# Optimization experiments

Hardware: AMD Instinct MI355X
Metric: run time of the kernel (lower is better)

## Reference

```python
import jax, jax.numpy as jnp
import numpy as np

EPS = 1e-6


def setup_inputs() -> dict:
    key = jax.random.key(0)
    kx, kw = jax.random.split(key)
    B, C, N = 8, 256, 2048
    x = jax.random.normal(kx, (B, C, N), dtype=jnp.float32)
    # nn.Linear(dim*2, 2, bias=False): weight shape [2, 2*C]
    W = jax.random.normal(kw, (2, 2 * C), dtype=jnp.float32) * (1.0 / np.sqrt(2 * C))
    return {"x": x, "W": W}


def reference(x, W):
    B, C, N = x.shape
    # cosine similarity matrix [B, N, N]
    sim = jnp.einsum('bcn,bcm->bnm', x, x)
    # torch: sqrt(sum(x^2 + 1e-6, dim=1)) -> eps added per-channel before sum
    norms = jnp.sqrt(jnp.sum(x * x + EPS, axis=1))            # [B, N]
    io_abs = sim / (norms[:, :, None] * norms[:, None, :])    # [B, N, N]
    # zero the diagonal (fill_diagonal_(0)) before argmax
    io_abs = io_abs * (1.0 - jnp.eye(N, dtype=io_abs.dtype))
    idx = jnp.argmax(io_abs, axis=2)                          # [B, N] nearest-neighbor per token
    # gather retrieved features: f_re[b, :, n] = x[b, :, idx[b, n]]
    f_re = jnp.take_along_axis(x, idx[:, None, :], axis=2)    # [B, C, N]
    # gated fusion
    fus = jnp.concatenate([x, f_re], axis=1).transpose(0, 2, 1)  # [B, N, 2C]
    w = jax.nn.softmax(fus @ W.T, axis=-1)                    # [B, N, 2]
    w = w.transpose(0, 2, 1)                                  # [B, 2, N]
    out = x * w[:, 0:1, :] + f_re * w[:, 1:2, :]
    return (out, f_re)
```

## Files before the change

kernel.cpp:

```cpp
#include <hip/hip_runtime.h>
#include <hip/hip_bf16.h>
#include <math.h>

constexpr int B_ = 8;
constexpr int C_ = 256;
constexpr int N_ = 2048;
constexpr int CN_ = C_ * N_;
constexpr int TOT_ = B_ * C_ * N_;
constexpr int BN_ = B_ * N_;
constexpr int NTILES = 16;
constexpr int NPAIRS = 136;
constexpr float EPSC = 256.0f * 1e-6f;

typedef __attribute__((ext_vector_type(8))) short bf16x8;
typedef __attribute__((ext_vector_type(4))) float f32x4;
typedef __attribute__((ext_vector_type(2))) unsigned int u32x2;

__device__ __forceinline__ void g2l16(const void* g, void* l) {
    __builtin_amdgcn_global_load_lds(
        (const __attribute__((address_space(1))) void*)g,
        (__attribute__((address_space(3))) void*)l, 16, 0, 0);
}

__device__ __forceinline__ unsigned short bits(__hip_bfloat16 h) {
    union { __hip_bfloat16 b; unsigned short u; } cv;
    cv.b = h;
    return cv.u;
}

__device__ __forceinline__ float b2f(short s) {
    union { float f; unsigned u; } cv;
    cv.u = ((unsigned)(unsigned short)s) << 16;
    return cv.f;
}

__device__ __forceinline__ unsigned long long packkey(float v, int m) {
    const unsigned b = __float_as_uint(v);
    const unsigned u = (b & 0x80000000u) ? ~b : (b | 0x80000000u);
    return ((unsigned long long)u << 32) | (unsigned)(2047 - m);
}

__device__ __forceinline__ float rnorm4(const float* __restrict__ normp, int idx) {
    return 1.0f / sqrtf(normp[idx] + EPSC);
}

__device__ __forceinline__ unsigned packpair(float a, float b) {
    return ((unsigned)bits(__float2bfloat16(b)) << 16) | bits(__float2bfloat16(a));
}

__global__ __launch_bounds__(256) void convert_kernel(const float* __restrict__ x,
                                                      __hip_bfloat16* __restrict__ hiT,
                                                      __hip_bfloat16* __restrict__ loT,
                                                      float* __restrict__ normp,
                                                      int* __restrict__ rcnt) {
    const int blk = blockIdx.x;
    const int batch = blk & 7;
    const int nt = (blk >> 3) & 31;
    const int ctile = blk >> 8;
    const int n0 = nt << 6, c0 = ctile << 6;
    const int t = threadIdx.x;

    if (blk == 0 && t == 0) rcnt[0] = 0;

    __shared__ float tb[64][65];
    __shared__ float red[16][65];

    const int i4 = t & 15;
    const int j = t >> 4;
    const float* xp = x + (size_t)batch * CN_ + (size_t)c0 * N_ + n0;
#pragma unroll
    for (int p = 0; p < 4; ++p) {
        const int cl = j + p * 16;
        const float4 v = *(const float4*)(xp + (size_t)cl * N_ + 4 * i4);
        tb[cl][4 * i4 + 0] = v.x;
        tb[cl][4 * i4 + 1] = v.y;
        tb[cl][4 * i4 + 2] = v.z;
        tb[cl][4 * i4 + 3] = v.w;
    }
    __syncthreads();

    const int cq = t & 15;
    const int nb = t >> 4;
    const int c = cq << 2;
#pragma unroll
    for (int r = 0; r < 4; ++r) {
        const int n = nb + r * 16;
        const float v0 = tb[c][n], v1 = tb[c + 1][n];
        const float v2 = tb[c + 2][n], v3 = tb[c + 3][n];
        const __hip_bfloat16 h0 = __float2bfloat16(v0);
        const __hip_bfloat16 h1 = __float2bfloat16(v1);
        const __hip_bfloat16 h2 = __float2bfloat16(v2);
        const __hip_bfloat16 h3 = __float2bfloat16(v3);
        const float g0 = v0 - __bfloat162float(h0);
        const float g1 = v1 - __bfloat162float(h1);
        const float g2 = v2 - __bfloat162float(h2);
        const float g3 = v3 - __bfloat162float(h3);
        red[cq][n] = v0 * v0 + v1 * v1 + v2 * v2 + v3 * v3;
        const size_t o = ((size_t)batch * N_ + n0 + n) * C_ + c0 + c;
        u32x2 hp, lp;
        hp[0] = ((unsigned)bits(h1) << 16) | bits(h0);
        hp[1] = ((unsigned)bits(h3) << 16) | bits(h2);
        lp[0] = packpair(g0, g1);
        lp[1] = packpair(g2, g3);
        ((u32x2*)hiT)[o >> 2] = hp;
        ((u32x2*)loT)[o >> 2] = lp;
        __syncthreads();
    }
    if (t < 64) {
        float s = 0.f;
#pragma unroll
        for (int g = 0; g < 16; ++g) s += red[g][t];
        normp[ctile * BN_ + batch * N_ + n0 + t] = s;
    }
}

__device__ __forceinline__ float rnormsum(const float* __restrict__ normp, int idx) {
    return 1.0f / sqrtf(normp[idx] + normp[BN_ + idx] + normp[2 * BN_ + idx] +
                        normp[3 * BN_ + idx] + EPSC);
}

__global__ __launch_bounds__(512) void gram_mfma_kernel(
        const __hip_bfloat16* __restrict__ hiT, const __hip_bfloat16* __restrict__ loT,
        const float* __restrict__ normp,
        float* __restrict__ pval, int* __restrict__ pidx, float* __restrict__ pval2) {
    const int blk = blockIdx.x;
    const int batch = blk & 7;
    int p = blk >> 3;
    int bn = 0;
    while (p >= NTILES - bn) { p -= NTILES - bn; ++bn; }
    const int bm = bn + p;
    const bool diag = (bn == bm);
    const int n0 = bn << 7, m0 = bm << 7;

    __shared__ short As0[128 * 64];
    __shared__ short As1[128 * 64];
    __shared__ short Bs0[128 * 64];
    __shared__ short Bs1[128 * 64];
    short* ov = &As0[0];
    float (*rv1)[4] = (float(*)[4])(ov + 0);
    int (*ri1)[4] = (int(*)[4])(ov + 1024);
    float (*rv2)[4] = (float(*)[4])(ov + 2048);
    float (*cv1)[2] = (float(*)[2])(ov + 3072);
    int (*ci1)[2] = (int(*)[2])(ov + 3584);
    float (*cv2)[2] = (float(*)[2])(ov + 4096);
    float* rnA = (float*)(ov + 4608);

    const int tid = threadIdx.x;
    const int l = tid & 63, w = tid >> 6;
    const int lm = l & 15, q = l >> 4;
    const int x7 = lm & 7;
    const int wn = (w >> 2) << 6;
    const int wm = (w & 3) << 5;

    const size_t bbase = (size_t)batch * CN_;
    const short* gA[2];
    const short* gB[2];
    int ldsoff[2];
#pragma unroll
    for (int pp = 0; pp < 2; ++pp) {
        const int slot = tid + pp * 512;
        const int r = slot >> 3, sidx = slot & 7;
        const int sw = sidx ^ (r & 7);
        const short* base = (const short*)((sw < 4) ? hiT : loT);
        gA[pp] = base + bbase + (size_t)(n0 + r) * C_ + (sw & 3) * 8;
        gB[pp] = base + bbase + (size_t)(m0 + r) * C_ + (sw & 3) * 8;
        ldsoff[pp] = slot * 8;
    }
    int aoff[8], boff[4];
#pragma unroll
    for (int rt = 0; rt < 4; ++rt) {
        const int ra = wn + rt * 16 + lm;
        aoff[rt * 2] = ra * 64 + ((q ^ x7) * 8);
        aoff[rt * 2 + 1] = ra * 64 + (((4 | q) ^ x7) * 8);
    }
#pragma unroll
    for (int ct = 0; ct < 2; ++ct) {
        const int rb = wm + ct * 16 + lm;
        boff[ct * 2] = rb * 64 + ((q ^ x7) * 8);
        boff[ct * 2 + 1] = rb * 64 + (((4 | q) ^ x7) * 8);
    }

    f32x4 acc[4][2];
#pragma unroll
    for (int rt = 0; rt < 4; ++rt)
#pragma unroll
        for (int ct = 0; ct < 2; ++ct) acc[rt][ct] = (f32x4){0.f, 0.f, 0.f, 0.f};

#pragma unroll
    for (int pp = 0; pp < 2; ++pp) {
        g2l16(gA[pp], As0 + ldsoff[pp]);
        g2l16(gB[pp], Bs0 + ldsoff[pp]);
    }
    __syncthreads();

#pragma unroll
    for (int kt = 0; kt < 8; ++kt) {
        short* Ac = (kt & 1) ? As1 : As0;
        short* Bc = (kt & 1) ? Bs1 : Bs0;
        if (kt < 7) {
            short* An = (kt & 1) ? As0 : As1;
            short* Bn = (kt & 1) ? Bs0 : Bs1;
#pragma unroll
            for (int pp = 0; pp < 2; ++pp) {
                g2l16(gA[pp] + (kt + 1) * 32, An + ldsoff[pp]);
                g2l16(gB[pp] + (kt + 1) * 32, Bn + ldsoff[pp]);
            }
        }
        bf16x8 ah[4], al[4], bh[2], bl[2];
#pragma unroll
        for (int rt = 0; rt < 4; ++rt) {
            ah[rt] = *(const bf16x8*)(Ac + aoff[rt * 2]);
            al[rt] = *(const bf16x8*)(Ac + aoff[rt * 2 + 1]);
        }
#pragma unroll
        for (int ct = 0; ct < 2; ++ct) {
            bh[ct] = *(const bf16x8*)(Bc + boff[ct * 2]);
            bl[ct] = *(const bf16x8*)(Bc + boff[ct * 2 + 1]);
        }
#pragma unroll
        for (int rt = 0; rt < 4; ++rt)
#pragma unroll
            for (int ct = 0; ct < 2; ++ct) {
                acc[rt][ct] = __builtin_amdgcn_mfma_f32_16x16x32_bf16(
                    ah[rt], bh[ct], acc[rt][ct], 0, 0, 0);
                acc[rt][ct] = __builtin_amdgcn_mfma_f32_16x16x32_bf16(
                    ah[rt], bl[ct], acc[rt][ct], 0, 0, 0);
                acc[rt][ct] = __builtin_amdgcn_mfma_f32_16x16x32_bf16(
                    al[rt], bh[ct], acc[rt][ct], 0, 0, 0);
            }
        __syncthreads();
    }

    if (tid < 128) rnA[tid] = rnormsum(normp, batch * N_ + n0 + tid);

    float rnm[2];
#pragma unroll
    for (int ct = 0; ct < 2; ++ct)
        rnm[ct] = rnormsum(normp, batch * N_ + m0 + wm + ct * 16 + lm);

#pragma unroll
    for (int rt = 0; rt < 4; ++rt) {
#pragma unroll
        for (int r = 0; r < 4; ++r) {
            const int nrow = n0 + wn + rt * 16 + q * 4 + r;
            float v1 = -3.4e38f, v2 = -3.4e38f;
            int i1 = 0x7fffffff;
#pragma unroll
            for (int ct = 0; ct < 2; ++ct) {
                const int m = m0 + wm + ct * 16 + lm;
                const float v = acc[rt][ct][r] * rnm[ct];
                if (m == nrow) continue;
                if (v > v1) { v2 = v1; v1 = v; i1 = m; }
                else if (v > v2) v2 = v;
            }
#pragma unroll
            for (int d = 1; d < 16; d <<= 1) {
                const float ov1 = __shfl_xor(v1, d, 64);
                const int oi1 = __shfl_xor(i1, d, 64);
                const float ov2 = __shfl_xor(v2, d, 64);
                if (ov1 > v1 || (ov1 == v1 && oi1 < i1)) {
                    v2 = fmaxf(v1, ov2); v1 = ov1; i1 = oi1;
                } else {
                    v2 = fmaxf(v2, ov1);
                }
            }
            if (lm == 0) {
                const int rloc = wn + rt * 16 + q * 4 + r;
                rv1[rloc][w & 3] = v1;
                ri1[rloc][w & 3] = i1;
                rv2[rloc][w & 3] = v2;
            }
        }
    }
    __syncthreads();

    if (!diag) {
        float rnn[4][4];
#pragma unroll
        for (int rt = 0; rt < 4; ++rt)
#pragma unroll
            for (int r = 0; r < 4; ++r) rnn[rt][r] = rnA[wn + rt * 16 + q * 4 + r];
#pragma unroll
        for (int ct = 0; ct < 2; ++ct) {
            float v1 = -3.4e38f, v2 = -3.4e38f;
            int i1 = 0x7fffffff;
#pragma unroll
            for (int rt = 0; rt < 4; ++rt) {
#pragma unroll
                for (int r = 0; r < 4; ++r) {
                    const float v = acc[rt][ct][r] * rnn[rt][r];
                    const int nn = n0 + wn + rt * 16 + q * 4 + r;
                    if (v > v1) { v2 = v1; v1 = v; i1 = nn; }
                    else if (v > v2) v2 = v;
                }
            }
#pragma unroll
            for (int d = 16; d < 64; d <<= 1) {
                const float ov1 = __shfl_xor(v1, d, 64);
                const int oi1 = __shfl_xor(i1, d, 64);
                const float ov2 = __shfl_xor(v2, d, 64);
                if (ov1 > v1 || (ov1 == v1 && oi1 < i1)) {
                    v2 = fmaxf(v1, ov2); v1 = ov1; i1 = oi1;
                } else {
                    v2 = fmaxf(v2, ov1);
                }
            }
            if (q == 0) {
                const int mloc = wm + ct * 16 + lm;
                cv1[mloc][w >> 2] = v1;
                ci1[mloc][w >> 2] = i1;
                cv2[mloc][w >> 2] = v2;
            }
        }
    }
    __syncthreads();

    if (tid < 128) {
        {
            float v1 = rv1[tid][0]; int i1 = ri1[tid][0]; float v2 = rv2[tid][0];
#pragma unroll
            for (int s = 1; s < 4; ++s) {
                const float ov1 = rv1[tid][s]; const int oi1 = ri1[tid][s]; const float ov2 = rv2[tid][s];
                if (ov1 > v1 || (ov1 == v1 && oi1 < i1)) { v2 = fmaxf(v1, ov2); v1 = ov1; i1 = oi1; }
                else v2 = fmaxf(v2, ov1);
            }
            const size_t gi = (size_t)(batch * NTILES + bm) * N_ + n0 + tid;
            pval[gi] = v1; pidx[gi] = i1; pval2[gi] = v2;
        }
        if (!diag) {
            float v1 = cv1[tid][0]; int i1 = ci1[tid][0]; float v2 = cv2[tid][0];
            const float ov1 = cv1[tid][1]; const int oi1 = ci1[tid][1]; const float ov2 = cv2[tid][1];
            if (ov1 > v1 || (ov1 == v1 && oi1 < i1)) { v2 = fmaxf(v1, ov2); v1 = ov1; i1 = oi1; }
            else v2 = fmaxf(v2, ov1);
            const size_t gi = (size_t)(batch * NTILES + bn) * N_ + m0 + tid;
            pval[gi] = v1; pidx[gi] = i1; pval2[gi] = v2;
        }
    }
}

__global__ void combine_kernel(const float* __restrict__ pval, const int* __restrict__ pidx,
                               const float* __restrict__ pval2, int* __restrict__ fidx,
                               int* __restrict__ rcnt, int* __restrict__ ridx,
                               unsigned long long* __restrict__ pbest) {
    const int gt = blockIdx.x * 256 + threadIdx.x;
    const int row = gt >> 2, part = gt & 3;
    const int batch = row >> 11, n = row & 2047;
    float v1 = -3.4e38f, v2 = -3.4e38f;
    int i1 = 0x7fffffff;
    for (int s = part; s < NTILES; s += 4) {
        const size_t gi = (size_t)(batch * NTILES + s) * N_ + n;
        const float ov1 = pval[gi]; const int oi1 = pidx[gi]; const float ov2 = pval2[gi];
        if (ov1 > v1 || (ov1 == v1 && oi1 < i1)) { v2 = fmaxf(v1, ov2); v1 = ov1; i1 = oi1; }
        else v2 = fmaxf(v2, ov1);
    }
#pragma unroll
    for (int d = 1; d < 4; d <<= 1) {
        const float ov1 = __shfl_xor(v1, d, 64);
        const int oi1 = __shfl_xor(i1, d, 64);
        const float ov2 = __shfl_xor(v2, d, 64);
        if (ov1 > v1 || (ov1 == v1 && oi1 < i1)) { v2 = fmaxf(v1, ov2); v1 = ov1; i1 = oi1; }
        else v2 = fmaxf(v2, ov1);
    }
    if (part == 0) {
        fidx[row] = i1;
        if (v1 - v2 < 4e-5f) {
            const int slot = atomicAdd(rcnt, 1);
            ridx[slot] = row;
            pbest[slot] = 0ull;
        }
    }
}

__global__ __launch_bounds__(256) void rescue_kernel(const float* __restrict__ x,
                                                     const float* __restrict__ normp,
                                                     const int* __restrict__ rcnt,
                                                     const int* __restrict__ ridx,
                                                     unsigned long long* __restrict__ pbest) {
    const int cnt = *rcnt;
    const int nwork = cnt << 3;
    const int tid = threadIdx.x;
    __shared__ unsigned long long bk[256];
    for (int wi = blockIdx.x; wi < nwork; wi += gridDim.x) {
        const int rr = wi >> 3, ch = wi & 7;
        const int t = ridx[rr];
        const int batch = t >> 11, n = t & 2047;
        const int m = (ch << 8) + tid;
        const float* xb = x + (size_t)batch * CN_;
        float s0 = 0.f, s1 = 0.f, s2 = 0.f, s3 = 0.f;
        const float* xn = xb + n;
        const float* xm = xb + m;
#pragma unroll 4
        for (int c = 0; c < C_; c += 4) {
            s0 += xn[(size_t)(c + 0) * N_] * xm[(size_t)(c + 0) * N_];
            s1 += xn[(size_t)(c + 1) * N_] * xm[(size_t)(c + 1) * N_];
            s2 += xn[(size_t)(c + 2) * N_] * xm[(size_t)(c + 2) * N_];
            s3 += xn[(size_t)(c + 3) * N_] * xm[(size_t)(c + 3) * N_];
        }
        const float v = ((s0 + s1) + (s2 + s3)) * rnormsum(normp, batch * N_ + m);
        bk[tid] = (m == n) ? 0ull : packkey(v, m);
        __syncthreads();
        for (int sft = 128; sft > 0; sft >>= 1) {
            if (tid < sft) {
                const unsigned long long o = bk[tid + sft];
                if (o > bk[tid]) bk[tid] = o;
            }
            __syncthreads();
        }
        if (tid == 0) atomicMax(&pbest[rr], bk[0]);
        __syncthreads();
    }
}

__global__ __launch_bounds__(512) void finish_kernel(const float* __restrict__ x,
                                                     const __hip_bfloat16* __restrict__ hiT,
                                                     const __hip_bfloat16* __restrict__ loT,
                                                     const float* __restrict__ W,
                                                     const int* __restrict__ fidx,
                                                     const int* __restrict__ rcnt,
                                                     const int* __restrict__ ridx,
                                                     const unsigned long long* __restrict__ pbest,
                                                     float* __restrict__ out) {
    const int batch = blockIdx.x & 7;
    const int nt = blockIdx.x >> 3;
    const int n0 = nt << 4;
    const int t = threadIdx.x;
    const int i = t & 15, cg = t >> 4;

    __shared__ float Wl[1024];
    __shared__ int il[16];
    __shared__ float pl0[32][17], pl1[32][17];
    __shared__ float w0s[16], w1s[16];

    for (int u = t; u < 1024; u += 512) Wl[u] = W[u];
    if (t < 16) il[t] = fidx[batch * N_ + n0 + t];
    __syncthreads();
    {
        const int cnt = *rcnt;
        for (int rr = t; rr < cnt; rr += 512) {
            const int tt = ridx[rr];
            if ((tt >> 11) == batch) {
                const int n = tt & 2047;
                if (n >= n0 && n < n0 + 16) {
                    const unsigned long long k = pbest[rr];
                    il[n - n0] = 2047 - (int)(unsigned)(k & 0xffffffffull);
                }
            }
        }
    }
    __syncthreads();

    const int myrow = il[i];
    const size_t rowb = ((size_t)batch * N_ + myrow) * C_ + cg * 8;

    float fre[8];
    {
        const bf16x8 h = *(const bf16x8*)(hiT + rowb);
        const bf16x8 g = *(const bf16x8*)(loT + rowb);
#pragma unroll
        for (int e = 0; e < 8; ++e) fre[e] = b2f(h[e]) + b2f(g[e]);
    }

    const float* xb = x + (size_t)batch * CN_ + n0 + i;
    float xr[8];
    float l0 = 0.f, l1 = 0.f;
#pragma unroll
    for (int cc = 0; cc < 8; ++cc) {
        const int c = cg * 8 + cc;
        const float xv = xb[(size_t)c * N_];
        xr[cc] = xv;
        l0 += xv * Wl[c] + fre[cc] * Wl[256 + c];
        l1 += xv * Wl[512 + c] + fre[cc] * Wl[768 + c];
    }
    pl0[cg][i] = l0;
    pl1[cg][i] = l1;
    __syncthreads();
    if (t < 16) {
        float L0 = 0.f, L1 = 0.f;
#pragma unroll
        for (int g = 0; g < 32; ++g) { L0 += pl0[g][t]; L1 += pl1[g][t]; }
        const float mx = fmaxf(L0, L1);
        const float e0 = expf(L0 - mx);
        const float e1 = expf(L1 - mx);
        const float inv = 1.0f / (e0 + e1);
        w0s[t] = e0 * inv;
        w1s[t] = e1 * inv;
    }
    __syncthreads();
    const float w0 = w0s[i], w1 = w1s[i];

#pragma unroll
    for (int cc = 0; cc < 8; ++cc) {
        const int c = cg * 8 + cc;
        const size_t off = (size_t)batch * CN_ + (size_t)c * N_ + n0 + i;
        __builtin_nontemporal_store(xr[cc] * w0 + fre[cc] * w1, out + off);
        __builtin_nontemporal_store(fre[cc], out + TOT_ + off);
    }
}

extern "C" void kernel_launch(void* const* d_in, const int* in_sizes, int n_in,
                              void* d_out, int out_size, void* d_ws, size_t ws_size,
                              hipStream_t stream) {
    const float* x = (const float*)d_in[0];
    const float* W = (const float*)d_in[1];
    float* out = (float*)d_out;

    const size_t BF_BYTES = (size_t)TOT_ * 2;
    const size_t NORM_BYTES = (size_t)BN_ * 4;
    const size_t P_BYTES = (size_t)B_ * NTILES * N_ * 4;

    uint8_t* p = (uint8_t*)d_ws;
    __hip_bfloat16* hiT = (__hip_bfloat16*)p; p += BF_BYTES;
    __hip_bfloat16* loT = (__hip_bfloat16*)p; p += BF_BYTES;
    float* normp = (float*)p; p += 4 * NORM_BYTES;
    float* pval = (float*)p; p += P_BYTES;
    int* pidx = (int*)p; p += P_BYTES;
    float* pval2 = (float*)p; p += P_BYTES;
    int* fidx = (int*)p; p += NORM_BYTES;
    int* rcnt = (int*)p; p += 256;
    int* ridx = (int*)p; p += NORM_BYTES;
    unsigned long long* pbest = (unsigned long long*)p; p += (size_t)BN_ * 8;

    convert_kernel<<<1024, 256, 0, stream>>>(x, hiT, loT, normp, rcnt);
    gram_mfma_kernel<<<B_ * NPAIRS, 512, 0, stream>>>(hiT, loT, normp, pval, pidx, pval2);
    combine_kernel<<<256, 256, 0, stream>>>(pval, pidx, pval2, fidx, rcnt, ridx, pbest);
    rescue_kernel<<<2048, 256, 0, stream>>>(x, normp, rcnt, ridx, pbest);
    finish_kernel<<<1024, 512, 0, stream>>>(x, hiT, loT, W, fidx, rcnt, ridx, pbest, out);
}
```

Before: 166.2 us.

## Enlarge Gram tiles to 256x256, drop double buffering, shuffle-reduce norms

Doubles the Gram block tile to 256x256 with a 128x64 per-warp sub-tile, cutting block count and partial argmax outputs so each loaded tile is reused more. Replaces the double-buffered async LDS prefetch with a single buffer and barriers on both sides of each k-step. The convert kernel now reduces per-column norms with wave shuffles instead of an LDS array and per-iteration barriers. Risks include lost load/compute overlap, higher register pressure and fewer blocks than CUs.

After: 192.5 us. 15.8% more time.

```diff
diff --git a/kernel.cpp b/kernel.cpp
--- a/kernel.cpp
+++ b/kernel.cpp
@@ -8,8 +8,8 @@
 constexpr int CN_ = C_ * N_;
 constexpr int TOT_ = B_ * C_ * N_;
 constexpr int BN_ = B_ * N_;
-constexpr int NTILES = 16;
-constexpr int NPAIRS = 136;
+constexpr int NT2 = 8;
+constexpr int NP2 = 36;
 constexpr float EPSC = 256.0f * 1e-6f;
 
 typedef __attribute__((ext_vector_type(8))) short bf16x8;
@@ -40,12 +40,13 @@
     return ((unsigned long long)u << 32) | (unsigned)(2047 - m);
 }
 
-__device__ __forceinline__ float rnorm4(const float* __restrict__ normp, int idx) {
-    return 1.0f / sqrtf(normp[idx] + EPSC);
-}
-
 __device__ __forceinline__ unsigned packpair(float a, float b) {
     return ((unsigned)bits(__float2bfloat16(b)) << 16) | bits(__float2bfloat16(a));
+}
+
+__device__ __forceinline__ float rnormsum(const float* __restrict__ normp, int idx) {
+    return 1.0f / sqrtf(normp[idx] + normp[BN_ + idx] + normp[2 * BN_ + idx] +
+                        normp[3 * BN_ + idx] + EPSC);
 }
 
 __global__ __launch_bounds__(256) void convert_kernel(const float* __restrict__ x,
@@ -63,7 +64,6 @@
     if (blk == 0 && t == 0) rcnt[0] = 0;
 
     __shared__ float tb[64][65];
-    __shared__ float red[16][65];
 
     const int i4 = t & 15;
     const int j = t >> 4;
@@ -95,7 +95,6 @@
         const float g1 = v1 - __bfloat162float(h1);
         const float g2 = v2 - __bfloat162float(h2);
         const float g3 = v3 - __bfloat162float(h3);
-        red[cq][n] = v0 * v0 + v1 * v1 + v2 * v2 + v3 * v3;
         const size_t o = ((size_t)batch * N_ + n0 + n) * C_ + c0 + c;
         u32x2 hp, lp;
         hp[0] = ((unsigned)bits(h1) << 16) | bits(h0);
@@ -104,19 +103,11 @@
         lp[1] = packpair(g2, g3);
         ((u32x2*)hiT)[o >> 2] = hp;
         ((u32x2*)loT)[o >> 2] = lp;
-        __syncthreads();
-    }
-    if (t < 64) {
-        float s = 0.f;
-#pragma unroll
-        for (int g = 0; g < 16; ++g) s += red[g][t];
-        normp[ctile * BN_ + batch * N_ + n0 + t] = s;
-    }
-}
-
-__device__ __forceinline__ float rnormsum(const float* __restrict__ normp, int idx) {
-    return 1.0f / sqrtf(normp[idx] + normp[BN_ + idx] + normp[2 * BN_ + idx] +
-                        normp[3 * BN_ + idx] + EPSC);
+        float nrm = v0 * v0 + v1 * v1 + v2 * v2 + v3 * v3;
+#pragma unroll
+        for (int d = 1; d < 16; d <<= 1) nrm += __shfl_xor(nrm, d, 64);
+        if (cq == 0) normp[ctile * BN_ + batch * N_ + n0 + n] = nrm;
+    }
 }
 
 __global__ __launch_bounds__(512) void gram_mfma_kernel(
@@ -127,37 +118,35 @@
     const int batch = blk & 7;
     int p = blk >> 3;
     int bn = 0;
-    while (p >= NTILES - bn) { p -= NTILES - bn; ++bn; }
+    while (p >= NT2 - bn) { p -= NT2 - bn; ++bn; }
     const int bm = bn + p;
     const bool diag = (bn == bm);
-    const int n0 = bn << 7, m0 = bm << 7;
-
-    __shared__ short As0[128 * 64];
-    __shared__ short As1[128 * 64];
-    __shared__ short Bs0[128 * 64];
-    __shared__ short Bs1[128 * 64];
-    short* ov = &As0[0];
+    const int n0 = bn << 8, m0 = bm << 8;
+
+    __shared__ short As[256 * 64];
+    __shared__ short Bs[256 * 64];
+    short* ov = &As[0];
     float (*rv1)[4] = (float(*)[4])(ov + 0);
-    int (*ri1)[4] = (int(*)[4])(ov + 1024);
-    float (*rv2)[4] = (float(*)[4])(ov + 2048);
-    float (*cv1)[2] = (float(*)[2])(ov + 3072);
-    int (*ci1)[2] = (int(*)[2])(ov + 3584);
-    float (*cv2)[2] = (float(*)[2])(ov + 4096);
-    float* rnA = (float*)(ov + 4608);
+    int (*ri1)[4] = (int(*)[4])(ov + 2048);
+    float (*rv2)[4] = (float(*)[4])(ov + 4096);
+    float (*cv1)[2] = (float(*)[2])(ov + 6144);
+    int (*ci1)[2] = (int(*)[2])(ov + 7168);
+    float (*cv2)[2] = (float(*)[2])(ov + 8192);
+    float* rnA = (float*)(ov + 9216);
 
     const int tid = threadIdx.x;
     const int l = tid & 63, w = tid >> 6;
     const int lm = l & 15, q = l >> 4;
     const int x7 = lm & 7;
-    const int wn = (w >> 2) << 6;
-    const int wm = (w & 3) << 5;
+    const int wn = (w >> 2) << 7;
+    const int wm = (w & 3) << 6;
 
     const size_t bbase = (size_t)batch * CN_;
-    const short* gA[2];
-    const short* gB[2];
-    int ldsoff[2];
-#pragma unroll
-    for (int pp = 0; pp < 2; ++pp) {
+    const short* gA[4];
+    const short* gB[4];
+    int ldsoff[4];
+#pragma unroll
+    for (int pp = 0; pp < 4; ++pp) {
         const int slot = tid + pp * 512;
         const int r = slot >> 3, sidx = slot & 7;
         const int sw = sidx ^ (r & 7);
@@ -166,87 +155,73 @@
         gB[pp] = base + bbase + (size_t)(m0 + r) * C_ + (sw & 3) * 8;
         ldsoff[pp] = slot * 8;
     }
-    int aoff[8], boff[4];
-#pragma unroll
-    for (int rt = 0; rt < 4; ++rt) {
+    int aoffh[8], aoffl[8], boffh[4], boffl[4];
+#pragma unroll
+    for (int rt = 0; rt < 8; ++rt) {
         const int ra = wn + rt * 16 + lm;
-        aoff[rt * 2] = ra * 64 + ((q ^ x7) * 8);
-        aoff[rt * 2 + 1] = ra * 64 + (((4 | q) ^ x7) * 8);
-    }
-#pragma unroll
-    for (int ct = 0; ct < 2; ++ct) {
+        aoffh[rt] = ra * 64 + ((q ^ x7) * 8);
+        aoffl[rt] = ra * 64 + (((4 | q) ^ x7) * 8);
+    }
+#pragma unroll
+    for (int ct = 0; ct < 4; ++ct) {
         const int rb = wm + ct * 16 + lm;
-        boff[ct * 2] = rb * 64 + ((q ^ x7) * 8);
-        boff[ct * 2 + 1] = rb * 64 + (((4 | q) ^ x7) * 8);
-    }
-
-    f32x4 acc[4][2];
-#pragma unroll
-    for (int rt = 0; rt < 4; ++rt)
-#pragma unroll
-        for (int ct = 0; ct < 2; ++ct) acc[rt][ct] = (f32x4){0.f, 0.f, 0.f, 0.f};
-
-#pragma unroll
-    for (int pp = 0; pp < 2; ++pp) {
-        g2l16(gA[pp], As0 + ldsoff[pp]);
-        g2l16(gB[pp], Bs0 + ldsoff[pp]);
-    }
-    __syncthreads();
-
-#pragma unroll
+        boffh[ct] = rb * 64 + ((q ^ x7) * 8);
+        boffl[ct] = rb * 64 + (((4 | q) ^ x7) * 8);
+    }
+
+    f32x4 acc[8][4];
+#pragma unroll
+    for (int rt = 0; rt < 8; ++rt)
+#pragma unroll
+        for (int ct = 0; ct < 4; ++ct) acc[rt][ct] = (f32x4){0.f, 0.f, 0.f, 0.f};
+
     for (int kt = 0; kt < 8; ++kt) {
-        short* Ac = (kt & 1) ? As1 : As0;
-        short* Bc = (kt & 1) ? Bs1 : Bs0;
-        if (kt < 7) {
-            short* An = (kt & 1) ? As0 : As1;
-            short* Bn = (kt & 1) ? Bs0 : Bs1;
-#pragma unroll
-            for (int pp = 0; pp < 2; ++pp) {
-                g2l16(gA[pp] + (kt + 1) * 32, An + ldsoff[pp]);
-                g2l16(gB[pp] + (kt + 1) * 32, Bn + ldsoff[pp]);
-            }
-        }
-        bf16x8 ah[4], al[4], bh[2], bl[2];
-#pragma unroll
-        for (int rt = 0; rt < 4; ++rt) {
-            ah[rt] = *(const bf16x8*)(Ac + aoff[rt * 2]);
-            al[rt] = *(const bf16x8*)(Ac + aoff[rt * 2 + 1]);
-        }
-#pragma unroll
-        for (int ct = 0; ct < 2; ++ct) {
-            bh[ct] = *(const bf16x8*)(Bc + boff[ct * 2]);
-            bl[ct] = *(const bf16x8*)(Bc + boff[ct * 2 + 1]);
-        }
-#pragma unroll
-        for (int rt = 0; rt < 4; ++rt)
-#pragma unroll
-            for (int ct = 0; ct < 2; ++ct) {
+        __syncthreads();
+#pragma unroll
+        for (int pp = 0; pp < 4; ++pp) {
+            g2l16(gA[pp] + kt * 32, As + ldsoff[pp]);
+            g2l16(gB[pp] + kt * 32, Bs + ldsoff[pp]);
+        }
+        __syncthreads();
+        bf16x8 bh[4], bl[4];
+#pragma unroll
+        for (int ct = 0; ct < 4; ++ct) {
+            bh[ct] = *(const bf16x8*)(Bs + boffh[ct]);
+            bl[ct] = *(const bf16x8*)(Bs + boffl[ct]);
+        }
+#pragma unroll
+        for (int rt = 0; rt < 8; ++rt) {
+            const bf16x8 ah = *(const bf16x8*)(As + aoffh[rt]);
+            const bf16x8 al = *(const bf16x8*)(As + aoffl[rt]);
+#pragma unroll
+            for (int ct = 0; ct < 4; ++ct) {
                 acc[rt][ct] = __builtin_amdgcn_mfma_f32_16x16x32_bf16(
-                    ah[rt], bh[ct], acc[rt][ct], 0, 0, 0);
+                    ah, bh[ct], acc[rt][ct], 0, 0, 0);
                 acc[rt][ct] = __builtin_amdgcn_mfma_f32_16x16x32_bf16(
-                    ah[rt], bl[ct], acc[rt][ct], 0, 0, 0);
+                    ah, bl[ct], acc[rt][ct], 0, 0, 0);
                 acc[rt][ct] = __builtin_amdgcn_mfma_f32_16x16x32_bf16(
-                    al[rt], bh[ct], acc[rt][ct], 0, 0, 0);
-            }
-        __syncthreads();
-    }
-
-    if (tid < 128) rnA[tid] = rnormsum(normp, batch * N_ + n0 + tid);
-
-    float rnm[2];
-#pragma unroll
-    for (int ct = 0; ct < 2; ++ct)
+                    al, bh[ct], acc[rt][ct], 0, 0, 0);
+            }
+        }
+    }
+    __syncthreads();
+
+    if (tid < 256) rnA[tid] = rnormsum(normp, batch * N_ + n0 + tid);
+
+    float rnm[4];
+#pragma unroll
+    for (int ct = 0; ct < 4; ++ct)
         rnm[ct] = rnormsum(normp, batch * N_ + m0 + wm + ct * 16 + lm);
 
 #pragma unroll
-    for (int rt = 0; rt < 4; ++rt) {
+    for (int rt = 0; rt < 8; ++rt) {
 #pragma unroll
         for (int r = 0; r < 4; ++r) {
             const int nrow = n0 + wn + rt * 16 + q * 4 + r;
             float v1 = -3.4e38f, v2 = -3.4e38f;
             int i1 = 0x7fffffff;
 #pragma unroll
-            for (int ct = 0; ct < 2; ++ct) {
+            for (int ct = 0; ct < 4; ++ct) {
                 const int m = m0 + wm + ct * 16 + lm;
                 const float v = acc[rt][ct][r] * rnm[ct];
                 if (m == nrow) continue;
@@ -275,20 +250,15 @@
     __syncthreads();
 
     if (!diag) {
-        float rnn[4][4];
-#pragma unroll
-        for (int rt = 0; rt < 4; ++rt)
-#pragma unroll
-            for (int r = 0; r < 4; ++r) rnn[rt][r] = rnA[wn + rt * 16 + q * 4 + r];
-#pragma unroll
-        for (int ct = 0; ct < 2; ++ct) {
+#pragma unroll
+        for (int ct = 0; ct < 4; ++ct) {
             float v1 = -3.4e38f, v2 = -3.4e38f;
             int i1 = 0x7fffffff;
 #pragma unroll
-            for (int rt = 0; rt < 4; ++rt) {
+            for (int rt = 0; rt < 8; ++rt) {
 #pragma unroll
                 for (int r = 0; r < 4; ++r) {
-                    const float v = acc[rt][ct][r] * rnn[rt][r];
+                    const float v = acc[rt][ct][r] * rnA[wn + rt * 16 + q * 4 + r];
                     const int nn = n0 + wn + rt * 16 + q * 4 + r;
                     if (v > v1) { v2 = v1; v1 = v; i1 = nn; }
                     else if (v > v2) v2 = v;
@@ -315,7 +285,7 @@
     }
     __syncthreads();
 
-    if (tid < 128) {
+    if (tid < 256) {
         {
             float v1 = rv1[tid][0]; int i1 = ri1[tid][0]; float v2 = rv2[tid][0];
 #pragma unroll
@@ -324,7 +294,7 @@
                 if (ov1 > v1 || (ov1 == v1 && oi1 < i1)) { v2 = fmaxf(v1, ov2); v1 = ov1; i1 = oi1; }
                 else v2 = fmaxf(v2, ov1);
             }
-            const size_t gi = (size_t)(batch * NTILES + bm) * N_ + n0 + tid;
+            const size_t gi = (size_t)(batch * NT2 + bm) * N_ + n0 + tid;
             pval[gi] = v1; pidx[gi] = i1; pval2[gi] = v2;
         }
         if (!diag) {
@@ -332,7 +302,7 @@
             const float ov1 = cv1[tid][1]; const int oi1 = ci1[tid][1]; const float ov2 = cv2[tid][1];
             if (ov1 > v1 || (ov1 == v1 && oi1 < i1)) { v2 = fmaxf(v1, ov2); v1 = ov1; i1 = oi1; }
             else v2 = fmaxf(v2, ov1);
-            const size_t gi = (size_t)(batch * NTILES + bn) * N_ + m0 + tid;
+            const size_t gi = (size_t)(batch * NT2 + bn) * N_ + m0 + tid;
             pval[gi] = v1; pidx[gi] = i1; pval2[gi] = v2;
         }
     }
@@ -347,8 +317,8 @@
     const int batch = row >> 11, n = row & 2047;
     float v1 = -3.4e38f, v2 = -3.4e38f;
     int i1 = 0x7fffffff;
-    for (int s = part; s < NTILES; s += 4) {
-        const size_t gi = (size_t)(batch * NTILES + s) * N_ + n;
+    for (int s = part; s < NT2; s += 4) {
+        const size_t gi = (size_t)(batch * NT2 + s) * N_ + n;
         const float ov1 = pval[gi]; const int oi1 = pidx[gi]; const float ov2 = pval2[gi];
         if (ov1 > v1 || (ov1 == v1 && oi1 < i1)) { v2 = fmaxf(v1, ov2); v1 = ov1; i1 = oi1; }
         else v2 = fmaxf(v2, ov1);
@@ -506,7 +476,7 @@
 
     const size_t BF_BYTES = (size_t)TOT_ * 2;
     const size_t NORM_BYTES = (size_t)BN_ * 4;
-    const size_t P_BYTES = (size_t)B_ * NTILES * N_ * 4;
+    const size_t P_BYTES = (size_t)B_ * NT2 * N_ * 4;
 
     uint8_t* p = (uint8_t*)d_ws;
     __hip_bfloat16* hiT = (__hip_bfloat16*)p; p += BF_BYTES;
@@ -521,7 +491,7 @@
     unsigned long long* pbest = (unsigned long long*)p; p += (size_t)BN_ * 8;
 
     convert_kernel<<<1024, 256, 0, stream>>>(x, hiT, loT, normp, rcnt);
-    gram_mfma_kernel<<<B_ * NPAIRS, 512, 0, stream>>>(hiT, loT, normp, pval, pidx, pval2);
+    gram_mfma_kernel<<<B_ * NP2, 512, 0, stream>>>(hiT, loT, normp, pval, pidx, pval2);
     combine_kernel<<<256, 256, 0, stream>>>(pval, pidx, pval2, fidx, rcnt, ridx, pbest);
     rescue_kernel<<<2048, 256, 0, stream>>>(x, normp, rcnt, ridx, pbest);
     finish_kernel<<<1024, 512, 0, stream>>>(x, hiT, loT, W, fidx, rcnt, ridx, pbest, out);
```
